# Kernel tuning notes

Hardware: AMD Instinct MI355X
Metric: run time of the kernel (lower is better)

The kernel has to match this reference:

```python
import jax, jax.numpy as jnp
import numpy as np

NQ = 10                      # num_qubits
B = 32768                    # batch
DIM = 2 ** NQ                # statevector dimension
U3_LAYERS = 2
ENT_LAYERS = 2
RING = [(i, (i + 1) % NQ) for i in range(NQ)]
EDGES = [RING, RING]         # one ring graph per entangling layer
N_WEIGHTS = 3 * NQ * U3_LAYERS + sum(len(e) for e in EDGES)  # 80

# PauliZ sign table: wire 0 is the most significant bit (PennyLane convention)
_idx = np.arange(DIM)
_SIGNS = np.stack([1.0 - 2.0 * ((_idx >> (NQ - 1 - q)) & 1) for q in range(NQ)],
                  axis=1).astype(np.float32)  # (DIM, NQ)


def _ry(theta):
    c = jnp.cos(theta / 2)
    s = jnp.sin(theta / 2)
    return jnp.stack([jnp.stack([c, -s], -1), jnp.stack([s, c], -1)], -2).astype(jnp.complex64)


def _rz(phi):
    em = jnp.exp(-0.5j * phi.astype(jnp.complex64))
    ep = jnp.exp(0.5j * phi.astype(jnp.complex64))
    z = jnp.zeros_like(em)
    return jnp.stack([jnp.stack([em, z], -1), jnp.stack([z, ep], -1)], -2)


def _rot(phi, theta, omega):
    # PennyLane Rot(phi, theta, omega) = RZ(omega) @ RY(theta) @ RZ(phi)
    return _rz(omega) @ _ry(theta) @ _rz(phi)


def _apply_1q(state, U, q):
    # state: (B, DIM); U: (2,2) shared or (B,2,2) per-sample
    L = 2 ** q
    R = DIM // (2 * L)
    s = state.reshape(-1, L, 2, R)
    if U.ndim == 3:
        out = jnp.einsum('bij,bljr->blir', U, s)
    else:
        out = jnp.einsum('ij,bljr->blir', U, s)
    return out.reshape(-1, DIM)


def _apply_cry(state, theta, u, v):
    # controlled-RY(theta): RY on target v where control u == 1
    t = state.reshape((-1,) + (2,) * NQ)
    s0 = jnp.take(t, 0, axis=u + 1)
    s1 = jnp.take(t, 1, axis=u + 1)
    ta = v + 1 if v < u else v  # target axis in slice after control axis removed
    s1m = jnp.moveaxis(s1, ta, -1)
    s1m = jnp.einsum('...j,ij->...i', s1m, _ry(theta))
    s1 = jnp.moveaxis(s1m, -1, ta)
    return jnp.stack([s0, s1], axis=u + 1).reshape(-1, DIM)


def _circuit(inputs, weights):
    # invert=True: angles = pi * clamp(inputs, 0, 1)
    ang = jnp.pi * jnp.clip(inputs, 0.0, 1.0)
    b = inputs.shape[0]
    state = jnp.zeros((b, DIM), jnp.complex64).at[:, 0].set(1.0)
    # AngleEmbedding with RY rotations (per-sample angles)
    for q in range(NQ):
        state = _apply_1q(state, _ry(ang[:, q]), q)
    w = 0
    for layer in range(max(U3_LAYERS, ENT_LAYERS)):
        if layer < U3_LAYERS:
            for q in range(NQ):
                state = _apply_1q(state, _rot(weights[w], weights[w + 1], weights[w + 2]), q)
                w += 3
        if layer < ENT_LAYERS:
            for (u, v) in EDGES[layer]:
                state = _apply_cry(state, weights[w], u, v)
                w += 1
    probs = state.real ** 2 + state.imag ** 2  # (B, DIM)
    return probs @ jnp.asarray(_SIGNS)         # (B, NQ) expval(PauliZ_q)


def setup_inputs() -> dict:
    key = jax.random.key(0)
    k1, k2 = jax.random.split(key)
    inputs = jax.random.uniform(k1, (B, NQ), dtype=jnp.float32)
    weights = jax.random.normal(k2, (N_WEIGHTS,), dtype=jnp.float32) * 0.1
    return {"inputs": inputs, "weights": weights}


def reference(inputs, weights):
    return _circuit(inputs, weights)
```

## Files before the change

### kernel.cpp

```cpp
#include <hip/hip_runtime.h>


namespace {

constexpr int NQB = 10;

typedef _Float16 h2 __attribute__((ext_vector_type(2)));

__device__ __forceinline__ float h2_as_f(h2 v) { return __builtin_bit_cast(float, v); }
__device__ __forceinline__ h2 f_as_h2(float v) { return __builtin_bit_cast(h2, v); }

__device__ __forceinline__ h2 pk2(float a, float b) {
#if __has_builtin(__builtin_amdgcn_cvt_pkrtz)
  return __builtin_bit_cast(h2, __builtin_amdgcn_cvt_pkrtz(a, b));
#else
  h2 r; r.x = (_Float16)a; r.y = (_Float16)b; return r;
#endif
}

__device__ __forceinline__ h2 hsplat(float f) {
  const _Float16 h = (_Float16)f;
  h2 r; r.x = h; r.y = h; return r;
}

__device__ __forceinline__ h2 hsel(bool c, h2 a, h2 b) {
  return f_as_h2(c ? h2_as_f(a) : h2_as_f(b));
}

template<int CTRL>
__device__ __forceinline__ float dppf(float x) {
  return __uint_as_float((unsigned)__builtin_amdgcn_update_dpp(
      0, (int)__float_as_uint(x), CTRL, 0xF, 0xF, true));
}

template<int P>
__device__ __forceinline__ float xorf(float x, int bpa) {
  if constexpr (P == 0) {
    return dppf<0xB1>(x);
  } else if constexpr (P == 1) {
    return dppf<0x4E>(x);
  } else if constexpr (P == 2) {
    return __uint_as_float((unsigned)__builtin_amdgcn_ds_swizzle(
        (int)__float_as_uint(x), 0x101F));
  } else if constexpr (P == 3) {
    return dppf<0x128>(x);
  } else if constexpr (P == 4) {
    return __uint_as_float((unsigned)__builtin_amdgcn_ds_swizzle(
        (int)__float_as_uint(x), 0x401F));
  } else {
    return __uint_as_float((unsigned)__builtin_amdgcn_ds_bpermute(
        bpa, (int)__float_as_uint(x)));
  }
}

template<int P>
__device__ __forceinline__ h2 xorh(h2 v, int bpa) {
  return f_as_h2(xorf<P>(h2_as_f(v), bpa));
}

__device__ __forceinline__ float fsin_rev(float rev) {
#if __has_builtin(__builtin_amdgcn_sinf)
  return __builtin_amdgcn_sinf(rev);
#else
  return __sinf(rev * 6.2831853071795864769f);
#endif
}
__device__ __forceinline__ float fcos_rev(float rev) {
#if __has_builtin(__builtin_amdgcn_cosf)
  return __builtin_amdgcn_cosf(rev);
#else
  return __cosf(rev * 6.2831853071795864769f);
#endif
}

__device__ __forceinline__ float clamp01(float x) {
#if __has_builtin(__builtin_amdgcn_fmed3f)
  return __builtin_amdgcn_fmed3f(x, 0.0f, 1.0f);
#else
  return fminf(fmaxf(x, 0.0f), 1.0f);
#endif
}

__device__ __forceinline__ void cmulf(float& r, float& i, float br, float bi) {
  const float tr = r * br - i * bi;
  i = r * bi + i * br;
  r = tr;
}

__device__ __forceinline__ void cmulh(h2& r, h2& i, h2 br, h2 bi) {
  const h2 tr = r*br - i*bi;
  i = r*bi + i*br;
  r = tr;
}

__device__ __forceinline__ void qubit_uv(const float* m, float x,
                                         float& u0r, float& u0i,
                                         float& u1r, float& u1i) {
  const float r = 0.25f * clamp01(x);
  const float fs = fsin_rev(r), fc = fcos_rev(r);
  u0r = m[0]*fc + m[2]*fs;  u0i = m[1]*fc + m[3]*fs;
  u1r = m[4]*fc + m[6]*fs;  u1i = m[5]*fc + m[7]*fs;
}

__device__ __forceinline__ void lane_fold_cry(const float* __restrict__ xin, int lane,
                                              const float (*gm)[8], const float (*gc0)[2],
                                              float& Lr, float& Li) {
  Lr = 1.0f; Li = 0.0f;
#pragma unroll
  for (int pt = 0; pt < 5; ++pt) {
    const int q = 9 - pt, e = 8 - pt;
    float u0r, u0i, u1r, u1i;
    qubit_uv(&gm[q][0], xin[q], u0r, u0i, u1r, u1i);
    const bool bt = (lane >> pt) & 1;
    const bool bc = (lane >> (pt + 1)) & 1;
    const float c = gc0[e][0];
    const float s = bt ? gc0[e][1] : -gc0[e][1];
    const float ubr = bt ? u1r : u0r, ubi = bt ? u1i : u0i;
    const float uor = bt ? u0r : u1r, uoi = bt ? u0i : u1i;
    const float vr = c*ubr + s*uor, vi = c*ubi + s*uoi;
    const float wr = bc ? vr : ubr, wi = bc ? vi : ubi;
    if (pt == 0) { Lr = wr; Li = wi; }
    else cmulf(Lr, Li, wr, wi);
  }
}

__device__ __forceinline__ void level_tab(const float* m, float c, float s,
                                          float xa, float xb,
                                          h2 (&wr)[4], h2 (&wi)[4]) {
  float a0r, a0i, a1r, a1i, b0r, b0i, b1r, b1i;
  qubit_uv(m, xa, a0r, a0i, a1r, a1i);
  qubit_uv(m, xb, b0r, b0i, b1r, b1i);
  const float va0r = c*a0r - s*a1r, va0i = c*a0i - s*a1i;
  const float va1r = s*a0r + c*a1r, va1i = s*a0i + c*a1i;
  const float vb0r = c*b0r - s*b1r, vb0i = c*b0i - s*b1i;
  const float vb1r = s*b0r + c*b1r, vb1i = s*b0i + c*b1i;
  wr[0] = pk2(a0r, b0r);  wi[0] = pk2(a0i, b0i);
  wr[1] = pk2(a1r, b1r);  wi[1] = pk2(a1i, b1i);
  wr[2] = pk2(va0r, vb0r); wi[2] = pk2(va0i, vb0i);
  wr[3] = pk2(va1r, vb1r); wi[3] = pk2(va1i, vb1i);
}


__device__ __forceinline__ void apply_diag16(h2 (&Hr)[16], h2 (&Hi)[16],
                                             h2 zr, h2 zi, const h2 (*zk)[2]) {
#pragma unroll
  for (int k = 0; k < 16; ++k) {
    const h2 kc = zk[k][0], ks = zk[k][1];
    const h2 cr = zr*kc - zi*ks;
    const h2 ci = zi*kc + zr*ks;
    const h2 tr = cr*Hr[k] - ci*Hi[k];
    const h2 ti = ci*Hr[k] + cr*Hi[k];
    Hr[k] = tr;  Hi[k] = ti;
  }
}

template<int J>
__device__ __forceinline__ void ry_reg16(h2 (&Hr)[16], h2 (&Hi)[16], h2 c, h2 s) {
#pragma unroll
  for (int k0 = 0; k0 < 16; ++k0) {
    if (k0 & J) continue;
    const int k1 = k0 | J;
    const h2 a0r = Hr[k0], a1r = Hr[k1], a0i = Hi[k0], a1i = Hi[k1];
    Hr[k0] = c*a0r - s*a1r;  Hr[k1] = s*a0r + c*a1r;
    Hi[k0] = c*a0i - s*a1i;  Hi[k1] = s*a0i + c*a1i;
  }
}

template<int P>
__device__ __forceinline__ void ry_lane16(h2 (&Hr)[16], h2 (&Hi)[16], h2 c, h2 ss,
                                          int bpa) {
#pragma unroll
  for (int k = 0; k < 16; ++k) {
    const h2 pr = xorh<P>(Hr[k], bpa);
    const h2 pi = xorh<P>(Hi[k], bpa);
    Hr[k] = c*Hr[k] + ss*pr;
    Hi[k] = c*Hi[k] + ss*pi;
  }
}

template<int CB, int J>
__device__ __forceinline__ void cry_rr(h2 (&Hr)[16], h2 (&Hi)[16], h2 c, h2 s) {
#pragma unroll
  for (int k0 = 0; k0 < 16; ++k0) {
    if ((k0 & J) || !(k0 & CB)) continue;
    const int k1 = k0 | J;
    const h2 a0r = Hr[k0], a1r = Hr[k1], a0i = Hi[k0], a1i = Hi[k1];
    Hr[k0] = c*a0r - s*a1r;  Hr[k1] = s*a0r + c*a1r;
    Hi[k0] = c*a0i - s*a1i;  Hi[k1] = s*a0i + c*a1i;
  }
}

__device__ __forceinline__ void cry_k0_l5(h2 (&Hr)[16], h2 (&Hi)[16], h2 c, h2 s,
                                          int lane, int bpa) {
  const h2 ss = hsel((lane >> 5) & 1, s, -s);
#pragma unroll
  for (int k = 1; k < 16; k += 2) {
    const h2 pr = xorh<5>(Hr[k], bpa);
    const h2 pi = xorh<5>(Hi[k], bpa);
    Hr[k] = c*Hr[k] + ss*pr;
    Hi[k] = c*Hi[k] + ss*pi;
  }
}

template<int PC, int PT>
__device__ __forceinline__ void cry_ll(h2 (&Hr)[16], h2 (&Hi)[16], h2 c, h2 s,
                                       h2 HONE, h2 HZERO, int lane, int bpa) {
  const bool ctrl = (lane >> PC) & 1;
  const h2 ce = hsel(ctrl, c, HONE);
  const h2 se = hsel(ctrl, s, HZERO);
  const h2 ss = hsel((lane >> PT) & 1, se, -se);
#pragma unroll
  for (int k = 0; k < 16; ++k) {
    const h2 pr = xorh<PT>(Hr[k], bpa);
    const h2 pi = xorh<PT>(Hi[k], bpa);
    Hr[k] = ce*Hr[k] + ss*pr;
    Hi[k] = ce*Hi[k] + ss*pi;
  }
}

__device__ __forceinline__ void cry_l0_r8(h2 (&Hr)[16], h2 (&Hi)[16], h2 c, h2 s,
                                          h2 HONE, h2 HZERO, int lane) {
  const bool ctrl = lane & 1;
  const h2 ce = hsel(ctrl, c, HONE);
  const h2 se = hsel(ctrl, s, HZERO);
#pragma unroll
  for (int k0 = 0; k0 < 8; ++k0) {
    const int k1 = k0 + 8;
    const h2 a0r = Hr[k0], a1r = Hr[k1], a0i = Hi[k0], a1i = Hi[k1];
    Hr[k0] = ce*a0r - se*a1r;  Hr[k1] = se*a0r + ce*a1r;
    Hi[k0] = ce*a0i - se*a1i;  Hi[k1] = se*a0i + ce*a1i;
  }
}

__device__ __forceinline__ void finish_sample(const float (&p)[16], int lane, int bpa,
                                              float* __restrict__ outp) {
  float t[8], T[4];
  float e6 = 0.0f;
#pragma unroll
  for (int j = 0; j < 8; ++j) { t[j] = p[2*j] + p[2*j+1]; e6 += p[2*j] - p[2*j+1]; }
  float e7 = 0.0f;
#pragma unroll
  for (int j = 0; j < 4; ++j) { T[j] = t[2*j] + t[2*j+1]; e7 += t[2*j] - t[2*j+1]; }
  const float U0 = T[0] + T[1], U1 = T[2] + T[3];
  const float e8 = (T[0] - T[1]) + (T[2] - T[3]);
  const float tot = U0 + U1;
  const float e9 = U0 - U1;

  float sgn[6];
#pragma unroll
  for (int q = 0; q < 6; ++q) sgn[q] = ((lane >> q) & 1) ? -1.0f : 1.0f;

  float E[6];
  float tt = tot;
#define QSTEP(P)                                                   \
  {                                                                \
    const float pt = xorf<P>(tt, bpa);                             \
    E[P] = sgn[P] * (tt - pt);                                     \
    tt += pt;                                                      \
    _Pragma("unroll")                                              \
    for (int jj = 0; jj < P; ++jj) E[jj] += xorf<P>(E[jj], bpa);   \
  }
  QSTEP(0) QSTEP(1) QSTEP(2) QSTEP(3) QSTEP(4) QSTEP(5)
#undef QSTEP

  float a6 = e6, a7 = e7, a8 = e8, a9 = e9;
#define RSTEP(P)                 \
  a6 += xorf<P>(a6, bpa);        \
  a7 += xorf<P>(a7, bpa);        \
  a8 += xorf<P>(a8, bpa);        \
  a9 += xorf<P>(a9, bpa);
  RSTEP(0) RSTEP(1) RSTEP(2) RSTEP(3) RSTEP(4) RSTEP(5)
#undef RSTEP

  if (lane < 10) {
    float v = a9;
    v = (lane == 1) ? a8 : v;
    v = (lane == 2) ? a7 : v;
    v = (lane == 3) ? a6 : v;
    v = (lane == 4) ? E[5] : v;
    v = (lane == 5) ? E[4] : v;
    v = (lane == 6) ? E[3] : v;
    v = (lane == 7) ? E[2] : v;
    v = (lane == 8) ? E[1] : v;
    v = (lane == 9) ? E[0] : v;
    outp[lane] = v;
  }
}

}

__global__ __launch_bounds__(256)
void qlayer_kernel(const float* __restrict__ inp,
                   const float* __restrict__ wt,
                   float* __restrict__ out,
                   int B)
{
  __shared__ float gm[10][8];
  __shared__ float gc0[10][2];
  __shared__ h2 gch1[10][2];
  __shared__ h2 grot1h[10][2];
  __shared__ h2 gdk[2][16][2];
  __shared__ float gzlane[2][64][2];

  const int tid = threadIdx.x;

  if (tid < 10) {
    const int w = 3 * tid;
    const float phi = wt[w], th = wt[w + 1], om = wt[w + 2];
    float s, c, sa, ca, sb, cb;
    __sincosf(0.5f * th, &s, &c);
    __sincosf(0.5f * (phi + om), &sa, &ca);
    __sincosf(0.5f * (phi - om), &sb, &cb);
    gm[tid][0] =  c * ca;  gm[tid][1] = -c * sa;
    gm[tid][2] = -s * cb;  gm[tid][3] = -s * sb;
    gm[tid][4] =  s * cb;  gm[tid][5] = -s * sb;
    gm[tid][6] =  c * ca;  gm[tid][7] =  c * sa;
  } else if (tid >= 16 && tid < 26) {
    const int e = tid - 16;
    float s, c;
    __sincosf(0.5f * wt[30 + e], &s, &c);
    gc0[e][0] = c;
    gc0[e][1] = s;
  } else if (tid >= 32 && tid < 42) {
    const int e = tid - 32;
    float s, c;
    __sincosf(0.5f * wt[70 + e], &s, &c);
    gch1[e][0] = hsplat(c);
    gch1[e][1] = hsplat(s);
  } else if (tid >= 48 && tid < 58) {
    const int q = tid - 48;
    float s, c;
    __sincosf(0.5f * wt[41 + 3 * q], &s, &c);
    grot1h[q][0] = hsplat(c);
    grot1h[q][1] = hsplat(s);
  } else if (tid >= 64 && tid < 96) {
    const int t = tid - 64;
    const int d = t >> 4, k = t & 15;
    const int wb = d ? 42 : 40;
    float ang = 0.0f;
    if (k & 1) ang += wt[wb + 9];
    if (k & 2) ang += wt[wb + 6];
    if (k & 4) ang += wt[wb + 3];
    if (k & 8) ang += wt[wb + 0];
    float s, c;
    __sincosf(ang, &s, &c);
    gdk[d][k][0] = hsplat(c);
    gdk[d][k][1] = hsplat(s);
  } else if (tid >= 128) {
    const int d = (tid - 128) >> 6, ln = tid & 63;
    const int wb = d ? 42 : 40;
    float ang = 0.0f;
    if (ln & 1)  ang += wt[wb + 27];
    if (ln & 2)  ang += wt[wb + 24];
    if (ln & 4)  ang += wt[wb + 21];
    if (ln & 8)  ang += wt[wb + 18];
    if (ln & 16) ang += wt[wb + 15];
    if (ln & 32) ang += wt[wb + 12];
    float s, c;
    __sincosf(ang, &s, &c);
    gzlane[d][ln][0] = c;
    gzlane[d][ln][1] = s;
  }
  __syncthreads();

  const int lane = tid & 63;
  const int bpa = (lane ^ 32) << 2;
  const int half = B >> 1;
  const int gw = blockIdx.x * 4 + (tid >> 6);
  if (gw >= half) return;
  const int sA = gw, sB = gw + half;
  const float* xA = inp + sA * NQB;
  const float* xB = inp + sB * NQB;

  const h2 HONE  = hsplat(1.0f);
  const h2 HZERO = hsplat(0.0f);


  float LrA, LiA, LrB, LiB;
  lane_fold_cry(xA, lane, gm, gc0, LrA, LiA);
  lane_fold_cry(xB, lane, gm, gc0, LrB, LiB);

  h2 W5ur, W5ui, W5vr, W5vi;
  {
    float a0r,a0i,a1r,a1i, b0r,b0i,b1r,b1i;
    qubit_uv(&gm[4][0], xA[4], a0r,a0i,a1r,a1i);
    qubit_uv(&gm[4][0], xB[4], b0r,b0i,b1r,b1i);
    const bool bt = (lane >> 5) & 1;
    const float c = gc0[3][0];
    const float s = bt ? gc0[3][1] : -gc0[3][1];
    const float uArr = bt ? a1r : a0r, uAri = bt ? a1i : a0i;
    const float uAor = bt ? a0r : a1r, uAoi = bt ? a0i : a1i;
    const float uBrr = bt ? b1r : b0r, uBri = bt ? b1i : b0i;
    const float uBor = bt ? b0r : b1r, uBoi = bt ? b0i : b1i;
    W5ur = pk2(uArr, uBrr);  W5ui = pk2(uAri, uBri);
    W5vr = pk2(c*uArr + s*uAor, c*uBrr + s*uBor);
    W5vi = pk2(c*uAri + s*uAoi, c*uBri + s*uBoi);
  }

  h2 Hr[16], Hi[16];
  {
    float a0r,a0i,a1r,a1i, b0r,b0i,b1r,b1i;
    qubit_uv(&gm[0][0], xA[0], a0r,a0i,a1r,a1i);
    qubit_uv(&gm[0][0], xB[0], b0r,b0i,b1r,b1i);
    float t0rA = LrA, t0iA = LiA;  cmulf(t0rA, t0iA, a0r, a0i);
    float t1rA = LrA, t1iA = LiA;  cmulf(t1rA, t1iA, a1r, a1i);
    float t0rB = LrB, t0iB = LiB;  cmulf(t0rB, t0iB, b0r, b0i);
    float t1rB = LrB, t1iB = LiB;  cmulf(t1rB, t1iB, b1r, b1i);
    Hr[0] = pk2(t0rA, t0rB);  Hi[0] = pk2(t0iA, t0iB);
    Hr[8] = pk2(t1rA, t1rB);  Hi[8] = pk2(t1iA, t1iB);
  }

  {
    h2 wr[4], wi[4];
    level_tab(&gm[1][0], gc0[0][0], gc0[0][1], xA[1], xB[1], wr, wi);
    Hr[4]  = Hr[0]; Hi[4]  = Hi[0]; cmulh(Hr[4],  Hi[4],  wr[1], wi[1]);
    cmulh(Hr[0],  Hi[0],  wr[0], wi[0]);
    Hr[12] = Hr[8]; Hi[12] = Hi[8]; cmulh(Hr[12], Hi[12], wr[3], wi[3]);
    cmulh(Hr[8],  Hi[8],  wr[2], wi[2]);
  }

  {
    h2 wr[4], wi[4];
    level_tab(&gm[2][0], gc0[1][0], gc0[1][1], xA[2], xB[2], wr, wi);
#pragma unroll
    for (int k = 0; k < 16; k += 4) {
      const int j = ((k >> 2) & 1) << 1;
      Hr[k+2] = Hr[k]; Hi[k+2] = Hi[k]; cmulh(Hr[k+2], Hi[k+2], wr[j|1], wi[j|1]);
      cmulh(Hr[k], Hi[k], wr[j], wi[j]);
    }
  }

  {
    h2 wr[4], wi[4];
    level_tab(&gm[3][0], gc0[2][0], gc0[2][1], xA[3], xB[3], wr, wi);
    cmulh(wr[0], wi[0], W5ur, W5ui);
    cmulh(wr[1], wi[1], W5vr, W5vi);
    cmulh(wr[2], wi[2], W5ur, W5ui);
    cmulh(wr[3], wi[3], W5vr, W5vi);
#pragma unroll
    for (int k = 0; k < 16; k += 2) {
      const int j = ((k >> 1) & 1) << 1;
      Hr[k+1] = Hr[k]; Hi[k+1] = Hi[k]; cmulh(Hr[k+1], Hi[k+1], wr[j|1], wi[j|1]);
      cmulh(Hr[k], Hi[k], wr[j], wi[j]);
    }
  }

  cry_l0_r8(Hr, Hi, hsplat(gc0[9][0]), hsplat(gc0[9][1]), HONE, HZERO, lane);

  {
    const float2 zp = *(const float2*)&gzlane[0][lane][0];
    apply_diag16(Hr, Hi, hsplat(zp.x), hsplat(zp.y), &gdk[0][0]);
    ry_reg16<8>(Hr, Hi, grot1h[0][0], grot1h[0][1]);
    ry_reg16<4>(Hr, Hi, grot1h[1][0], grot1h[1][1]);
    ry_reg16<2>(Hr, Hi, grot1h[2][0], grot1h[2][1]);
    ry_reg16<1>(Hr, Hi, grot1h[3][0], grot1h[3][1]);
    {
      const h2 s5 = grot1h[4][1];
      ry_lane16<5>(Hr, Hi, grot1h[4][0], hsel((lane >> 5) & 1, s5, -s5), bpa);
      const h2 s4 = grot1h[5][1];
      ry_lane16<4>(Hr, Hi, grot1h[5][0], hsel((lane >> 4) & 1, s4, -s4), bpa);
      const h2 s3 = grot1h[6][1];
      ry_lane16<3>(Hr, Hi, grot1h[6][0], hsel((lane >> 3) & 1, s3, -s3), bpa);
      const h2 s2 = grot1h[7][1];
      ry_lane16<2>(Hr, Hi, grot1h[7][0], hsel((lane >> 2) & 1, s2, -s2), bpa);
      const h2 s1 = grot1h[8][1];
      ry_lane16<1>(Hr, Hi, grot1h[8][0], hsel((lane >> 1) & 1, s1, -s1), bpa);
      const h2 s0 = grot1h[9][1];
      ry_lane16<0>(Hr, Hi, grot1h[9][0], hsel(lane & 1, s0, -s0), bpa);
    }
    const float2 zo = *(const float2*)&gzlane[1][lane][0];
    apply_diag16(Hr, Hi, hsplat(zo.x), hsplat(zo.y), &gdk[1][0]);

    const h2 (*cc)[2] = &gch1[0];
    cry_rr<8, 4>(Hr, Hi, cc[0][0], cc[0][1]);
    cry_rr<4, 2>(Hr, Hi, cc[1][0], cc[1][1]);
    cry_rr<2, 1>(Hr, Hi, cc[2][0], cc[2][1]);
    cry_k0_l5   (Hr, Hi, cc[3][0], cc[3][1], lane, bpa);
    cry_ll<5, 4>(Hr, Hi, cc[4][0], cc[4][1], HONE, HZERO, lane, bpa);
    cry_ll<4, 3>(Hr, Hi, cc[5][0], cc[5][1], HONE, HZERO, lane, bpa);
    cry_ll<3, 2>(Hr, Hi, cc[6][0], cc[6][1], HONE, HZERO, lane, bpa);
    cry_ll<2, 1>(Hr, Hi, cc[7][0], cc[7][1], HONE, HZERO, lane, bpa);
    cry_ll<1, 0>(Hr, Hi, cc[8][0], cc[8][1], HONE, HZERO, lane, bpa);
    cry_l0_r8   (Hr, Hi, cc[9][0], cc[9][1], HONE, HZERO, lane);
  }

  float pA[16], pB[16];
#pragma unroll
  for (int k = 0; k < 16; ++k) {
    const float rA = (float)Hr[k].x, rB = (float)Hr[k].y;
    const float iA = (float)Hi[k].x, iB = (float)Hi[k].y;
    pA[k] = rA * rA + iA * iA;
    pB[k] = rB * rB + iB * iB;
  }
  finish_sample(pA, lane, bpa, out + sA * NQB);
  finish_sample(pB, lane, bpa, out + sB * NQB);
}

extern "C" void kernel_launch(void* const* d_in, const int* in_sizes, int n_in,
                              void* d_out, int out_size, void* d_ws, size_t ws_size,
                              hipStream_t stream) {
  const float* inp = (const float*)d_in[0];
  const float* wt  = (const float*)d_in[1];
  float* out = (float*)d_out;
  const int B = in_sizes[0] / NQB;
  const int pairs = B / 2;
  const int nblocks = (pairs + 3) / 4;
  hipLaunchKernelGGL(qlayer_kernel, dim3(nblocks), dim3(256), 0, stream,
                     inp, wt, out, B);
}
```

Measured before the change: 81.32 us.

## Process two sample pairs per wave and vectorize final reduction over pair

Halves the grid so each wave loops over two sample pairs, spreading the per-block shared-memory gate-table setup across twice the work. It also merges the two per-sample final reductions into one pass on float2 vectors, so the two samples' cross-lane shuffles can be interleaved for more instruction-level parallelism. The cost is fewer waves available to hide latency and possibly more register pressure.

```diff
diff --git a/kernel.cpp b/kernel.cpp
--- a/kernel.cpp
+++ b/kernel.cpp
@@ -6,6 +6,7 @@
 constexpr int NQB = 10;
 
 typedef _Float16 h2 __attribute__((ext_vector_type(2)));
+typedef float v2f __attribute__((ext_vector_type(2)));
 
 __device__ __forceinline__ float h2_as_f(h2 v) { return __builtin_bit_cast(float, v); }
 __device__ __forceinline__ h2 f_as_h2(float v) { return __builtin_bit_cast(h2, v); }
@@ -58,6 +59,14 @@
   return f_as_h2(xorf<P>(h2_as_f(v), bpa));
 }
 
+template<int P>
+__device__ __forceinline__ v2f xor2(v2f v, int bpa) {
+  v2f r;
+  r.x = xorf<P>(v.x, bpa);
+  r.y = xorf<P>(v.y, bpa);
+  return r;
+}
+
 __device__ __forceinline__ float fsin_rev(float rev) {
 #if __has_builtin(__builtin_amdgcn_sinf)
   return __builtin_amdgcn_sinf(rev);
@@ -232,48 +241,49 @@
   }
 }
 
-__device__ __forceinline__ void finish_sample(const float (&p)[16], int lane, int bpa,
-                                              float* __restrict__ outp) {
-  float t[8], T[4];
-  float e6 = 0.0f;
+__device__ __forceinline__ void finish_pair(const v2f (&p)[16], int lane, int bpa,
+                                            float* __restrict__ outA,
+                                            float* __restrict__ outB) {
+  v2f t[8], T[4];
+  v2f e6 = {0.0f, 0.0f};
 #pragma unroll
   for (int j = 0; j < 8; ++j) { t[j] = p[2*j] + p[2*j+1]; e6 += p[2*j] - p[2*j+1]; }
-  float e7 = 0.0f;
+  v2f e7 = {0.0f, 0.0f};
 #pragma unroll
   for (int j = 0; j < 4; ++j) { T[j] = t[2*j] + t[2*j+1]; e7 += t[2*j] - t[2*j+1]; }
-  const float U0 = T[0] + T[1], U1 = T[2] + T[3];
-  const float e8 = (T[0] - T[1]) + (T[2] - T[3]);
-  const float tot = U0 + U1;
-  const float e9 = U0 - U1;
+  const v2f U0 = T[0] + T[1], U1 = T[2] + T[3];
+  const v2f e8 = (T[0] - T[1]) + (T[2] - T[3]);
+  const v2f tot = U0 + U1;
+  const v2f e9 = U0 - U1;
 
   float sgn[6];
 #pragma unroll
   for (int q = 0; q < 6; ++q) sgn[q] = ((lane >> q) & 1) ? -1.0f : 1.0f;
 
-  float E[6];
-  float tt = tot;
+  v2f E[6];
+  v2f tt = tot;
 #define QSTEP(P)                                                   \
   {                                                                \
-    const float pt = xorf<P>(tt, bpa);                             \
-    E[P] = sgn[P] * (tt - pt);                                     \
+    const v2f pt = xor2<P>(tt, bpa);                               \
+    E[P] = (tt - pt) * sgn[P];                                     \
     tt += pt;                                                      \
     _Pragma("unroll")                                              \
-    for (int jj = 0; jj < P; ++jj) E[jj] += xorf<P>(E[jj], bpa);   \
+    for (int jj = 0; jj < P; ++jj) E[jj] += xor2<P>(E[jj], bpa);   \
   }
   QSTEP(0) QSTEP(1) QSTEP(2) QSTEP(3) QSTEP(4) QSTEP(5)
 #undef QSTEP
 
-  float a6 = e6, a7 = e7, a8 = e8, a9 = e9;
+  v2f a6 = e6, a7 = e7, a8 = e8, a9 = e9;
 #define RSTEP(P)                 \
-  a6 += xorf<P>(a6, bpa);        \
-  a7 += xorf<P>(a7, bpa);        \
-  a8 += xorf<P>(a8, bpa);        \
-  a9 += xorf<P>(a9, bpa);
+  a6 += xor2<P>(a6, bpa);        \
+  a7 += xor2<P>(a7, bpa);        \
+  a8 += xor2<P>(a8, bpa);        \
+  a9 += xor2<P>(a9, bpa);
   RSTEP(0) RSTEP(1) RSTEP(2) RSTEP(3) RSTEP(4) RSTEP(5)
 #undef RSTEP
 
   if (lane < 10) {
-    float v = a9;
+    v2f v = a9;
     v = (lane == 1) ? a8 : v;
     v = (lane == 2) ? a7 : v;
     v = (lane == 3) ? a6 : v;
@@ -283,7 +293,8 @@
     v = (lane == 7) ? E[2] : v;
     v = (lane == 8) ? E[1] : v;
     v = (lane == 9) ? E[0] : v;
-    outp[lane] = v;
+    outA[lane] = v.x;
+    outB[lane] = v.y;
   }
 }
 
@@ -367,133 +378,138 @@
   const int bpa = (lane ^ 32) << 2;
   const int half = B >> 1;
   const int gw = blockIdx.x * 4 + (tid >> 6);
-  if (gw >= half) return;
-  const int sA = gw, sB = gw + half;
-  const float* xA = inp + sA * NQB;
-  const float* xB = inp + sB * NQB;
+  const int pstride = gridDim.x * 4;
 
   const h2 HONE  = hsplat(1.0f);
   const h2 HZERO = hsplat(0.0f);
 
-
-  float LrA, LiA, LrB, LiB;
-  lane_fold_cry(xA, lane, gm, gc0, LrA, LiA);
-  lane_fold_cry(xB, lane, gm, gc0, LrB, LiB);
-
-  h2 W5ur, W5ui, W5vr, W5vi;
-  {
-    float a0r,a0i,a1r,a1i, b0r,b0i,b1r,b1i;
-    qubit_uv(&gm[4][0], xA[4], a0r,a0i,a1r,a1i);
-    qubit_uv(&gm[4][0], xB[4], b0r,b0i,b1r,b1i);
-    const bool bt = (lane >> 5) & 1;
-    const float c = gc0[3][0];
-    const float s = bt ? gc0[3][1] : -gc0[3][1];
-    const float uArr = bt ? a1r : a0r, uAri = bt ? a1i : a0i;
-    const float uAor = bt ? a0r : a1r, uAoi = bt ? a0i : a1i;
-    const float uBrr = bt ? b1r : b0r, uBri = bt ? b1i : b0i;
-    const float uBor = bt ? b0r : b1r, uBoi = bt ? b0i : b1i;
-    W5ur = pk2(uArr, uBrr);  W5ui = pk2(uAri, uBri);
-    W5vr = pk2(c*uArr + s*uAor, c*uBrr + s*uBor);
-    W5vi = pk2(c*uAri + s*uAoi, c*uBri + s*uBoi);
-  }
-
-  h2 Hr[16], Hi[16];
-  {
-    float a0r,a0i,a1r,a1i, b0r,b0i,b1r,b1i;
-    qubit_uv(&gm[0][0], xA[0], a0r,a0i,a1r,a1i);
-    qubit_uv(&gm[0][0], xB[0], b0r,b0i,b1r,b1i);
-    float t0rA = LrA, t0iA = LiA;  cmulf(t0rA, t0iA, a0r, a0i);
-    float t1rA = LrA, t1iA = LiA;  cmulf(t1rA, t1iA, a1r, a1i);
-    float t0rB = LrB, t0iB = LiB;  cmulf(t0rB, t0iB, b0r, b0i);
-    float t1rB = LrB, t1iB = LiB;  cmulf(t1rB, t1iB, b1r, b1i);
-    Hr[0] = pk2(t0rA, t0rB);  Hi[0] = pk2(t0iA, t0iB);
-    Hr[8] = pk2(t1rA, t1rB);  Hi[8] = pk2(t1iA, t1iB);
-  }
-
-  {
-    h2 wr[4], wi[4];
-    level_tab(&gm[1][0], gc0[0][0], gc0[0][1], xA[1], xB[1], wr, wi);
-    Hr[4]  = Hr[0]; Hi[4]  = Hi[0]; cmulh(Hr[4],  Hi[4],  wr[1], wi[1]);
-    cmulh(Hr[0],  Hi[0],  wr[0], wi[0]);
-    Hr[12] = Hr[8]; Hi[12] = Hi[8]; cmulh(Hr[12], Hi[12], wr[3], wi[3]);
-    cmulh(Hr[8],  Hi[8],  wr[2], wi[2]);
-  }
-
-  {
-    h2 wr[4], wi[4];
-    level_tab(&gm[2][0], gc0[1][0], gc0[1][1], xA[2], xB[2], wr, wi);
-#pragma unroll
-    for (int k = 0; k < 16; k += 4) {
-      const int j = ((k >> 2) & 1) << 1;
-      Hr[k+2] = Hr[k]; Hi[k+2] = Hi[k]; cmulh(Hr[k+2], Hi[k+2], wr[j|1], wi[j|1]);
-      cmulh(Hr[k], Hi[k], wr[j], wi[j]);
-    }
-  }
-
-  {
-    h2 wr[4], wi[4];
-    level_tab(&gm[3][0], gc0[2][0], gc0[2][1], xA[3], xB[3], wr, wi);
-    cmulh(wr[0], wi[0], W5ur, W5ui);
-    cmulh(wr[1], wi[1], W5vr, W5vi);
-    cmulh(wr[2], wi[2], W5ur, W5ui);
-    cmulh(wr[3], wi[3], W5vr, W5vi);
-#pragma unroll
-    for (int k = 0; k < 16; k += 2) {
-      const int j = ((k >> 1) & 1) << 1;
-      Hr[k+1] = Hr[k]; Hi[k+1] = Hi[k]; cmulh(Hr[k+1], Hi[k+1], wr[j|1], wi[j|1]);
-      cmulh(Hr[k], Hi[k], wr[j], wi[j]);
-    }
-  }
-
-  cry_l0_r8(Hr, Hi, hsplat(gc0[9][0]), hsplat(gc0[9][1]), HONE, HZERO, lane);
-
-  {
-    const float2 zp = *(const float2*)&gzlane[0][lane][0];
-    apply_diag16(Hr, Hi, hsplat(zp.x), hsplat(zp.y), &gdk[0][0]);
-    ry_reg16<8>(Hr, Hi, grot1h[0][0], grot1h[0][1]);
-    ry_reg16<4>(Hr, Hi, grot1h[1][0], grot1h[1][1]);
-    ry_reg16<2>(Hr, Hi, grot1h[2][0], grot1h[2][1]);
-    ry_reg16<1>(Hr, Hi, grot1h[3][0], grot1h[3][1]);
+#pragma unroll 1
+  for (int j = 0; j < 2; ++j) {
+    const int pair = gw + j * pstride;
+    if (pair >= half) break;
+    const int sA = pair, sB = pair + half;
+    const float* xA = inp + sA * NQB;
+    const float* xB = inp + sB * NQB;
+
+
+    float LrA, LiA, LrB, LiB;
+    lane_fold_cry(xA, lane, gm, gc0, LrA, LiA);
+    lane_fold_cry(xB, lane, gm, gc0, LrB, LiB);
+
+    h2 W5ur, W5ui, W5vr, W5vi;
     {
-      const h2 s5 = grot1h[4][1];
-      ry_lane16<5>(Hr, Hi, grot1h[4][0], hsel((lane >> 5) & 1, s5, -s5), bpa);
-      const h2 s4 = grot1h[5][1];
-      ry_lane16<4>(Hr, Hi, grot1h[5][0], hsel((lane >> 4) & 1, s4, -s4), bpa);
-      const h2 s3 = grot1h[6][1];
-      ry_lane16<3>(Hr, Hi, grot1h[6][0], hsel((lane >> 3) & 1, s3, -s3), bpa);
-      const h2 s2 = grot1h[7][1];
-      ry_lane16<2>(Hr, Hi, grot1h[7][0], hsel((lane >> 2) & 1, s2, -s2), bpa);
-      const h2 s1 = grot1h[8][1];
-      ry_lane16<1>(Hr, Hi, grot1h[8][0], hsel((lane >> 1) & 1, s1, -s1), bpa);
-      const h2 s0 = grot1h[9][1];
-      ry_lane16<0>(Hr, Hi, grot1h[9][0], hsel(lane & 1, s0, -s0), bpa);
-    }
-    const float2 zo = *(const float2*)&gzlane[1][lane][0];
-    apply_diag16(Hr, Hi, hsplat(zo.x), hsplat(zo.y), &gdk[1][0]);
-
-    const h2 (*cc)[2] = &gch1[0];
-    cry_rr<8, 4>(Hr, Hi, cc[0][0], cc[0][1]);
-    cry_rr<4, 2>(Hr, Hi, cc[1][0], cc[1][1]);
-    cry_rr<2, 1>(Hr, Hi, cc[2][0], cc[2][1]);
-    cry_k0_l5   (Hr, Hi, cc[3][0], cc[3][1], lane, bpa);
-    cry_ll<5, 4>(Hr, Hi, cc[4][0], cc[4][1], HONE, HZERO, lane, bpa);
-    cry_ll<4, 3>(Hr, Hi, cc[5][0], cc[5][1], HONE, HZERO, lane, bpa);
-    cry_ll<3, 2>(Hr, Hi, cc[6][0], cc[6][1], HONE, HZERO, lane, bpa);
-    cry_ll<2, 1>(Hr, Hi, cc[7][0], cc[7][1], HONE, HZERO, lane, bpa);
-    cry_ll<1, 0>(Hr, Hi, cc[8][0], cc[8][1], HONE, HZERO, lane, bpa);
-    cry_l0_r8   (Hr, Hi, cc[9][0], cc[9][1], HONE, HZERO, lane);
-  }
-
-  float pA[16], pB[16];
-#pragma unroll
-  for (int k = 0; k < 16; ++k) {
-    const float rA = (float)Hr[k].x, rB = (float)Hr[k].y;
-    const float iA = (float)Hi[k].x, iB = (float)Hi[k].y;
-    pA[k] = rA * rA + iA * iA;
-    pB[k] = rB * rB + iB * iB;
-  }
-  finish_sample(pA, lane, bpa, out + sA * NQB);
-  finish_sample(pB, lane, bpa, out + sB * NQB);
+      float a0r,a0i,a1r,a1i, b0r,b0i,b1r,b1i;
+      qubit_uv(&gm[4][0], xA[4], a0r,a0i,a1r,a1i);
+      qubit_uv(&gm[4][0], xB[4], b0r,b0i,b1r,b1i);
+      const bool bt = (lane >> 5) & 1;
+      const float c = gc0[3][0];
+      const float s = bt ? gc0[3][1] : -gc0[3][1];
+      const float uArr = bt ? a1r : a0r, uAri = bt ? a1i : a0i;
+      const float uAor = bt ? a0r : a1r, uAoi = bt ? a0i : a1i;
+      const float uBrr = bt ? b1r : b0r, uBri = bt ? b1i : b0i;
+      const float uBor = bt ? b0r : b1r, uBoi = bt ? b0i : b1i;
+      W5ur = pk2(uArr, uBrr);  W5ui = pk2(uAri, uBri);
+      W5vr = pk2(c*uArr + s*uAor, c*uBrr + s*uBor);
+      W5vi = pk2(c*uAri + s*uAoi, c*uBri + s*uBoi);
+    }
+
+    h2 Hr[16], Hi[16];
+    {
+      float a0r,a0i,a1r,a1i, b0r,b0i,b1r,b1i;
+      qubit_uv(&gm[0][0], xA[0], a0r,a0i,a1r,a1i);
+      qubit_uv(&gm[0][0], xB[0], b0r,b0i,b1r,b1i);
+      float t0rA = LrA, t0iA = LiA;  cmulf(t0rA, t0iA, a0r, a0i);
+      float t1rA = LrA, t1iA = LiA;  cmulf(t1rA, t1iA, a1r, a1i);
+      float t0rB = LrB, t0iB = LiB;  cmulf(t0rB, t0iB, b0r, b0i);
+      float t1rB = LrB, t1iB = LiB;  cmulf(t1rB, t1iB, b1r, b1i);
+      Hr[0] = pk2(t0rA, t0rB);  Hi[0] = pk2(t0iA, t0iB);
+      Hr[8] = pk2(t1rA, t1rB);  Hi[8] = pk2(t1iA, t1iB);
+    }
+
+    {
+      h2 wr[4], wi[4];
+      level_tab(&gm[1][0], gc0[0][0], gc0[0][1], xA[1], xB[1], wr, wi);
+      Hr[4]  = Hr[0]; Hi[4]  = Hi[0]; cmulh(Hr[4],  Hi[4],  wr[1], wi[1]);
+      cmulh(Hr[0],  Hi[0],  wr[0], wi[0]);
+      Hr[12] = Hr[8]; Hi[12] = Hi[8]; cmulh(Hr[12], Hi[12], wr[3], wi[3]);
+      cmulh(Hr[8],  Hi[8],  wr[2], wi[2]);
+    }
+
+    {
+      h2 wr[4], wi[4];
+      level_tab(&gm[2][0], gc0[1][0], gc0[1][1], xA[2], xB[2], wr, wi);
+#pragma unroll
+      for (int k = 0; k < 16; k += 4) {
+        const int jj = ((k >> 2) & 1) << 1;
+        Hr[k+2] = Hr[k]; Hi[k+2] = Hi[k]; cmulh(Hr[k+2], Hi[k+2], wr[jj|1], wi[jj|1]);
+        cmulh(Hr[k], Hi[k], wr[jj], wi[jj]);
+      }
+    }
+
+    {
+      h2 wr[4], wi[4];
+      level_tab(&gm[3][0], gc0[2][0], gc0[2][1], xA[3], xB[3], wr, wi);
+      cmulh(wr[0], wi[0], W5ur, W5ui);
+      cmulh(wr[1], wi[1], W5vr, W5vi);
+      cmulh(wr[2], wi[2], W5ur, W5ui);
+      cmulh(wr[3], wi[3], W5vr, W5vi);
+#pragma unroll
+      for (int k = 0; k < 16; k += 2) {
+        const int jj = ((k >> 1) & 1) << 1;
+        Hr[k+1] = Hr[k]; Hi[k+1] = Hi[k]; cmulh(Hr[k+1], Hi[k+1], wr[jj|1], wi[jj|1]);
+        cmulh(Hr[k], Hi[k], wr[jj], wi[jj]);
+      }
+    }
+
+    cry_l0_r8(Hr, Hi, hsplat(gc0[9][0]), hsplat(gc0[9][1]), HONE, HZERO, lane);
+
+    {
+      const float2 zp = *(const float2*)&gzlane[0][lane][0];
+      apply_diag16(Hr, Hi, hsplat(zp.x), hsplat(zp.y), &gdk[0][0]);
+      ry_reg16<8>(Hr, Hi, grot1h[0][0], grot1h[0][1]);
+      ry_reg16<4>(Hr, Hi, grot1h[1][0], grot1h[1][1]);
+      ry_reg16<2>(Hr, Hi, grot1h[2][0], grot1h[2][1]);
+      ry_reg16<1>(Hr, Hi, grot1h[3][0], grot1h[3][1]);
+      {
+        const h2 s5 = grot1h[4][1];
+        ry_lane16<5>(Hr, Hi, grot1h[4][0], hsel((lane >> 5) & 1, s5, -s5), bpa);
+        const h2 s4 = grot1h[5][1];
+        ry_lane16<4>(Hr, Hi, grot1h[5][0], hsel((lane >> 4) & 1, s4, -s4), bpa);
+        const h2 s3 = grot1h[6][1];
+        ry_lane16<3>(Hr, Hi, grot1h[6][0], hsel((lane >> 3) & 1, s3, -s3), bpa);
+        const h2 s2 = grot1h[7][1];
+        ry_lane16<2>(Hr, Hi, grot1h[7][0], hsel((lane >> 2) & 1, s2, -s2), bpa);
+        const h2 s1 = grot1h[8][1];
+        ry_lane16<1>(Hr, Hi, grot1h[8][0], hsel((lane >> 1) & 1, s1, -s1), bpa);
+        const h2 s0 = grot1h[9][1];
+        ry_lane16<0>(Hr, Hi, grot1h[9][0], hsel(lane & 1, s0, -s0), bpa);
+      }
+      const float2 zo = *(const float2*)&gzlane[1][lane][0];
+      apply_diag16(Hr, Hi, hsplat(zo.x), hsplat(zo.y), &gdk[1][0]);
+
+      const h2 (*cc)[2] = &gch1[0];
+      cry_rr<8, 4>(Hr, Hi, cc[0][0], cc[0][1]);
+      cry_rr<4, 2>(Hr, Hi, cc[1][0], cc[1][1]);
+      cry_rr<2, 1>(Hr, Hi, cc[2][0], cc[2][1]);
+      cry_k0_l5   (Hr, Hi, cc[3][0], cc[3][1], lane, bpa);
+      cry_ll<5, 4>(Hr, Hi, cc[4][0], cc[4][1], HONE, HZERO, lane, bpa);
+      cry_ll<4, 3>(Hr, Hi, cc[5][0], cc[5][1], HONE, HZERO, lane, bpa);
+      cry_ll<3, 2>(Hr, Hi, cc[6][0], cc[6][1], HONE, HZERO, lane, bpa);
+      cry_ll<2, 1>(Hr, Hi, cc[7][0], cc[7][1], HONE, HZERO, lane, bpa);
+      cry_ll<1, 0>(Hr, Hi, cc[8][0], cc[8][1], HONE, HZERO, lane, bpa);
+      cry_l0_r8   (Hr, Hi, cc[9][0], cc[9][1], HONE, HZERO, lane);
+    }
+
+    v2f p2[16];
+#pragma unroll
+    for (int k = 0; k < 16; ++k) {
+      const float rA = (float)Hr[k].x, rB = (float)Hr[k].y;
+      const float iA = (float)Hi[k].x, iB = (float)Hi[k].y;
+      v2f v; v.x = rA * rA + iA * iA; v.y = rB * rB + iB * iB;
+      p2[k] = v;
+    }
+    finish_pair(p2, lane, bpa, out + sA * NQB, out + sB * NQB);
+  }
 }
 
 extern "C" void kernel_launch(void* const* d_in, const int* in_sizes, int n_in,
@@ -503,8 +519,8 @@
   const float* wt  = (const float*)d_in[1];
   float* out = (float*)d_out;
   const int B = in_sizes[0] / NQB;
-  const int pairs = B / 2;
-  const int nblocks = (pairs + 3) / 4;
+  const int waves = B / 4;
+  const int nblocks = (waves + 3) / 4;
   hipLaunchKernelGGL(qlayer_kernel, dim3(nblocks), dim3(256), 0, stream,
                      inp, wt, out, B);
 }
```

Measured after the change: 161.0 us. 98.0% more time.
